# Optimization experiments

Measured on AMD Instinct MI355X. Metric: run time of the kernel, lower is better.

Reference implementation:

```python
import jax, jax.numpy as jnp
import numpy as np

B, N = 8192, 2048


def setup_inputs() -> dict:
    key = jax.random.key(0)
    k1, k2 = jax.random.split(key)
    predictions = jax.random.normal(k1, (B, N), dtype=jnp.float32)
    targets = jax.random.normal(k2, (B, N), dtype=jnp.float32)
    return {"predictions": predictions, "targets": targets}


def reference(predictions, targets):
    # Original: per-batch NxN squared-difference cost matrix + scipy Hungarian,
    # then MSE(pred, optimally-permuted targets), averaged over the batch.
    # For scalar entries with cost (p_i - t_j)^2 the optimal assignment is the
    # monotone matching (rearrangement inequality): sort both vectors and pair
    # in order. This computes the exact same loss, fully vectorized.
    p_sorted = jnp.sort(predictions, axis=-1)  # [B, N]
    t_sorted = jnp.sort(targets, axis=-1)      # [B, N]
    # mean over N per row, then mean over B == global mean
    return jnp.mean((p_sorted - t_sorted) ** 2)
```

## Files before the change

kernel.cpp:

```cpp
#include <hip/hip_runtime.h>
#include <math.h>

#define ROWS 8192
#define NCOL 2048
#define V 32
#define THREADS 256

__device__ __forceinline__ void ce(float& a, float& b) {
  const float lo = fminf(a, b);
  const float hi = fmaxf(a, b);
  a = lo; b = hi;
}

__device__ __forceinline__ float ce_dir(float a, float b, float cdir) {
  return __builtin_amdgcn_fmed3f(a, b, cdir);
}

template <int CTRL>
__device__ __forceinline__ float dpp_mov(float x) {
  return __builtin_bit_cast(
      float, __builtin_amdgcn_update_dpp(0, __builtin_bit_cast(int, x),
                                         CTRL, 0xF, 0xF, true));
}

template <int PAT>
__device__ __forceinline__ float swz(float x) {
  return __builtin_bit_cast(
      float, __builtin_amdgcn_ds_swizzle(__builtin_bit_cast(int, x), PAT));
}

template <int M>
__device__ __forceinline__ float lane_xor(float x, int a63) {
  if constexpr (M == 1)       return dpp_mov<0xB1>(x);
  else if constexpr (M == 2)  return dpp_mov<0x4E>(x);
  else if constexpr (M == 3)  return dpp_mov<0x1B>(x);
  else if constexpr (M == 7)  return dpp_mov<0x141>(x);
  else if constexpr (M == 8)  return dpp_mov<0x128>(x);
  else if constexpr (M == 15) return dpp_mov<0x140>(x);
  else if constexpr (M == 4)  return swz<0x101F>(x);
  else if constexpr (M == 16) return swz<0x401F>(x);
  else if constexpr (M == 31) return swz<0x7C1F>(x);
  else {
    return __builtin_bit_cast(
        float, __builtin_amdgcn_ds_bpermute(a63, __builtin_bit_cast(int, x)));
  }
}

template <int M>
__device__ __forceinline__ void xpass1(float (&x)[V], float cdir, int a63) {
#pragma unroll
  for (int c = 0; c < V; c += 8) {
    float o[8];
#pragma unroll
    for (int u = 0; u < 8; ++u) o[u] = lane_xor<M>(x[c + u], a63);
#pragma unroll
    for (int u = 0; u < 8; ++u) x[c + u] = ce_dir(x[c + u], o[u], cdir);
  }
}

template <int KB>
__device__ __forceinline__ void merge1(float (&x)[V], int lane, int a63) {
  {
    constexpr int LM = 2 * KB - 1;
    const float cdir = (lane & KB) ? INFINITY : -INFINITY;
#pragma unroll
    for (int q = 0; q < 4; ++q) {
      const int vA = 4 * q;
      float o[8];
#pragma unroll
      for (int u = 0; u < 4; ++u) {
        o[u]     = lane_xor<LM>(x[(vA + u) ^ 31], a63);
        o[u + 4] = lane_xor<LM>(x[vA + u], a63);
      }
#pragma unroll
      for (int u = 0; u < 4; ++u) {
        x[vA + u]        = ce_dir(x[vA + u],        o[u],     cdir);
        x[(vA + u) ^ 31] = ce_dir(x[(vA + u) ^ 31], o[u + 4], cdir);
      }
    }
  }
  if constexpr (KB >= 32) xpass1<16>(x, (lane & 16) ? INFINITY : -INFINITY, a63);
  if constexpr (KB >= 16) xpass1<8>(x, (lane & 8) ? INFINITY : -INFINITY, a63);
  if constexpr (KB >= 8)  xpass1<4>(x, (lane & 4) ? INFINITY : -INFINITY, a63);
  if constexpr (KB >= 4)  xpass1<2>(x, (lane & 2) ? INFINITY : -INFINITY, a63);
  if constexpr (KB >= 2)  xpass1<1>(x, (lane & 1) ? INFINITY : -INFINITY, a63);
#pragma unroll
  for (int j = 16; j >= 1; j >>= 1) {
#pragma unroll
    for (int v = 0; v < V; ++v) {
      if ((v & j) == 0) ce(x[v], x[v | j]);
    }
  }
}

__device__ __forceinline__ void sort_one(float (&x)[V], int lane, int a63) {
#pragma unroll
  for (int k = 2; k <= V; k <<= 1) {
#pragma unroll
    for (int v = 0; v < V; ++v) {
      if ((v & (k >> 1)) == 0) ce(x[v], x[v ^ (k - 1)]);
    }
#pragma unroll
    for (int j = k >> 2; j >= 1; j >>= 1) {
#pragma unroll
      for (int v = 0; v < V; ++v) {
        if ((v & j) == 0) ce(x[v], x[v | j]);
      }
    }
  }
  merge1<1>(x, lane, a63);
  merge1<2>(x, lane, a63);
  merge1<4>(x, lane, a63);
  merge1<8>(x, lane, a63);
  merge1<16>(x, lane, a63);
  merge1<32>(x, lane, a63);
}

__global__ __launch_bounds__(THREADS, 6) void sort_mse_kernel(
    const float* __restrict__ pred, const float* __restrict__ targ,
    float* __restrict__ out) {
  const int lane = threadIdx.x & 63;
  const int wave = threadIdx.x >> 6;
  const int pair = wave & 1;
  const int role = wave >> 1;
  const int row = blockIdx.x * 2 + pair;
  const size_t base = (size_t)row * NCOL + (size_t)lane * V;
  const int a63 = ((lane ^ 63) << 2);

  __shared__ float tbuf[2][NCOL];

  float x[V];
  const float4* s4 = (const float4*)((role ? targ : pred) + base);
#pragma unroll
  for (int q = 0; q < V / 4; ++q) {
    const float4 a = s4[q];
    x[4 * q + 0] = a.x; x[4 * q + 1] = a.y;
    x[4 * q + 2] = a.z; x[4 * q + 3] = a.w;
  }

  sort_one(x, lane, a63);

  if (role == 1) {
#pragma unroll
    for (int q = 0; q < V / 4; ++q) {
      const int w = lane * V + 4 * (q ^ (lane & 7));
      *(float4*)&tbuf[pair][w] =
          make_float4(x[4 * q + 0], x[4 * q + 1], x[4 * q + 2], x[4 * q + 3]);
    }
  }
  __syncthreads();
  if (role == 1) return;

  float acc = 0.f;
#pragma unroll
  for (int q = 0; q < V / 4; ++q) {
    const int w = lane * V + 4 * (q ^ (lane & 7));
    const float4 t4 = *(const float4*)&tbuf[pair][w];
    float d;
    d = x[4 * q + 0] - t4.x; acc = fmaf(d, d, acc);
    d = x[4 * q + 1] - t4.y; acc = fmaf(d, d, acc);
    d = x[4 * q + 2] - t4.z; acc = fmaf(d, d, acc);
    d = x[4 * q + 3] - t4.w; acc = fmaf(d, d, acc);
  }
#pragma unroll
  for (int off = 32; off > 0; off >>= 1) acc += __shfl_down(acc, off, 64);
  if (lane == 0) {
    unsafeAtomicAdd(out, acc * (1.0f / ((float)ROWS * (float)NCOL)));
  }
}

extern "C" void kernel_launch(void* const* d_in, const int* in_sizes, int n_in,
                              void* d_out, int out_size, void* d_ws, size_t ws_size,
                              hipStream_t stream) {
  const float* pred = (const float*)d_in[0];
  const float* targ = (const float*)d_in[1];
  float* out = (float*)d_out;

  hipMemsetAsync(out, 0, sizeof(float), stream);
  sort_mse_kernel<<<ROWS / 2, THREADS, 0, stream>>>(pred, targ, out);
}
```

Baseline: 233.4 us.

## Split each row sort across two waves with 16 values per lane

Each row is now sorted by two waves instead of one, so every lane holds 16 values rather than 32. The final cross-wave bitonic merge stage exchanges data through LDS, followed by lane-xor passes that include a new xor-32 bpermute. Grid size doubles to one row per block, and the launch bound rises to 8 to raise occupancy through lower register pressure. The cost is extra LDS traffic and an additional block barrier per row.

```diff
diff --git a/kernel.cpp b/kernel.cpp
--- a/kernel.cpp
+++ b/kernel.cpp
@@ -3,7 +3,7 @@
 
 #define ROWS 8192
 #define NCOL 2048
-#define V 32
+#define V 16
 #define THREADS 256
 
 __device__ __forceinline__ void ce(float& a, float& b) {
@@ -30,7 +30,7 @@
 }
 
 template <int M>
-__device__ __forceinline__ float lane_xor(float x, int a63) {
+__device__ __forceinline__ float lane_xor(float x, int a32, int a63) {
   if constexpr (M == 1)       return dpp_mov<0xB1>(x);
   else if constexpr (M == 2)  return dpp_mov<0x4E>(x);
   else if constexpr (M == 3)  return dpp_mov<0x1B>(x);
@@ -40,52 +40,57 @@
   else if constexpr (M == 4)  return swz<0x101F>(x);
   else if constexpr (M == 16) return swz<0x401F>(x);
   else if constexpr (M == 31) return swz<0x7C1F>(x);
-  else {
+  else if constexpr (M == 32) {
+    return __builtin_bit_cast(
+        float, __builtin_amdgcn_ds_bpermute(a32, __builtin_bit_cast(int, x)));
+  } else {
     return __builtin_bit_cast(
         float, __builtin_amdgcn_ds_bpermute(a63, __builtin_bit_cast(int, x)));
   }
 }
 
 template <int M>
-__device__ __forceinline__ void xpass1(float (&x)[V], float cdir, int a63) {
+__device__ __forceinline__ void xpass(float (&x)[V], float cdir,
+                                      int a32, int a63) {
 #pragma unroll
   for (int c = 0; c < V; c += 8) {
     float o[8];
 #pragma unroll
-    for (int u = 0; u < 8; ++u) o[u] = lane_xor<M>(x[c + u], a63);
+    for (int u = 0; u < 8; ++u) o[u] = lane_xor<M>(x[c + u], a32, a63);
 #pragma unroll
     for (int u = 0; u < 8; ++u) x[c + u] = ce_dir(x[c + u], o[u], cdir);
   }
 }
 
-template <int KB>
-__device__ __forceinline__ void merge1(float (&x)[V], int lane, int a63) {
+template <int S>
+__device__ __forceinline__ void mergeS(float (&x)[V], int lane,
+                                       int a32, int a63) {
   {
-    constexpr int LM = 2 * KB - 1;
-    const float cdir = (lane & KB) ? INFINITY : -INFINITY;
-#pragma unroll
-    for (int q = 0; q < 4; ++q) {
+    constexpr int LM = 2 * S - 1;
+    const float cdir = (lane & S) ? INFINITY : -INFINITY;
+#pragma unroll
+    for (int q = 0; q < 2; ++q) {
       const int vA = 4 * q;
       float o[8];
 #pragma unroll
       for (int u = 0; u < 4; ++u) {
-        o[u]     = lane_xor<LM>(x[(vA + u) ^ 31], a63);
-        o[u + 4] = lane_xor<LM>(x[vA + u], a63);
+        o[u]     = lane_xor<LM>(x[(vA + u) ^ 15], a32, a63);
+        o[u + 4] = lane_xor<LM>(x[vA + u], a32, a63);
       }
 #pragma unroll
       for (int u = 0; u < 4; ++u) {
         x[vA + u]        = ce_dir(x[vA + u],        o[u],     cdir);
-        x[(vA + u) ^ 31] = ce_dir(x[(vA + u) ^ 31], o[u + 4], cdir);
+        x[(vA + u) ^ 15] = ce_dir(x[(vA + u) ^ 15], o[u + 4], cdir);
       }
     }
   }
-  if constexpr (KB >= 32) xpass1<16>(x, (lane & 16) ? INFINITY : -INFINITY, a63);
-  if constexpr (KB >= 16) xpass1<8>(x, (lane & 8) ? INFINITY : -INFINITY, a63);
-  if constexpr (KB >= 8)  xpass1<4>(x, (lane & 4) ? INFINITY : -INFINITY, a63);
-  if constexpr (KB >= 4)  xpass1<2>(x, (lane & 2) ? INFINITY : -INFINITY, a63);
-  if constexpr (KB >= 2)  xpass1<1>(x, (lane & 1) ? INFINITY : -INFINITY, a63);
-#pragma unroll
-  for (int j = 16; j >= 1; j >>= 1) {
+  if constexpr (S >= 32) xpass<16>(x, (lane & 16) ? INFINITY : -INFINITY, a32, a63);
+  if constexpr (S >= 16) xpass<8>(x, (lane & 8) ? INFINITY : -INFINITY, a32, a63);
+  if constexpr (S >= 8)  xpass<4>(x, (lane & 4) ? INFINITY : -INFINITY, a32, a63);
+  if constexpr (S >= 4)  xpass<2>(x, (lane & 2) ? INFINITY : -INFINITY, a32, a63);
+  if constexpr (S >= 2)  xpass<1>(x, (lane & 1) ? INFINITY : -INFINITY, a32, a63);
+#pragma unroll
+  for (int j = 8; j >= 1; j >>= 1) {
 #pragma unroll
     for (int v = 0; v < V; ++v) {
       if ((v & j) == 0) ce(x[v], x[v | j]);
@@ -93,79 +98,114 @@
   }
 }
 
-__device__ __forceinline__ void sort_one(float (&x)[V], int lane, int a63) {
-#pragma unroll
-  for (int k = 2; k <= V; k <<= 1) {
-#pragma unroll
-    for (int v = 0; v < V; ++v) {
-      if ((v & (k >> 1)) == 0) ce(x[v], x[v ^ (k - 1)]);
-    }
-#pragma unroll
-    for (int j = k >> 2; j >= 1; j >>= 1) {
-#pragma unroll
-      for (int v = 0; v < V; ++v) {
-        if ((v & j) == 0) ce(x[v], x[v | j]);
-      }
-    }
-  }
-  merge1<1>(x, lane, a63);
-  merge1<2>(x, lane, a63);
-  merge1<4>(x, lane, a63);
-  merge1<8>(x, lane, a63);
-  merge1<16>(x, lane, a63);
-  merge1<32>(x, lane, a63);
-}
-
-__global__ __launch_bounds__(THREADS, 6) void sort_mse_kernel(
+__global__ __launch_bounds__(THREADS, 8) void sort_mse_kernel(
     const float* __restrict__ pred, const float* __restrict__ targ,
     float* __restrict__ out) {
   const int lane = threadIdx.x & 63;
   const int wave = threadIdx.x >> 6;
-  const int pair = wave & 1;
+  const int wp = wave & 1;
   const int role = wave >> 1;
-  const int row = blockIdx.x * 2 + pair;
-  const size_t base = (size_t)row * NCOL + (size_t)lane * V;
+  const int row = blockIdx.x;
+  const size_t base = (size_t)row * NCOL + (size_t)(wp * 64 + lane) * V;
+  const int a32 = ((lane ^ 32) << 2);
   const int a63 = ((lane ^ 63) << 2);
-
-  __shared__ float tbuf[2][NCOL];
+  const int swl = (lane ^ (lane >> 2)) & 3;
+
+  __shared__ float lds[4][64][V];
 
   float x[V];
   const float4* s4 = (const float4*)((role ? targ : pred) + base);
 #pragma unroll
-  for (int q = 0; q < V / 4; ++q) {
+  for (int q = 0; q < 4; ++q) {
     const float4 a = s4[q];
     x[4 * q + 0] = a.x; x[4 * q + 1] = a.y;
     x[4 * q + 2] = a.z; x[4 * q + 3] = a.w;
   }
 
-  sort_one(x, lane, a63);
-
+#pragma unroll
+  for (int k = 2; k <= V; k <<= 1) {
+#pragma unroll
+    for (int v = 0; v < V; ++v) {
+      if ((v & (k >> 1)) == 0) ce(x[v], x[v ^ (k - 1)]);
+    }
+#pragma unroll
+    for (int j = k >> 2; j >= 1; j >>= 1) {
+#pragma unroll
+      for (int v = 0; v < V; ++v) {
+        if ((v & j) == 0) ce(x[v], x[v | j]);
+      }
+    }
+  }
+
+  mergeS<1>(x, lane, a32, a63);
+  mergeS<2>(x, lane, a32, a63);
+  mergeS<4>(x, lane, a32, a63);
+  mergeS<8>(x, lane, a32, a63);
+  mergeS<16>(x, lane, a32, a63);
+  mergeS<32>(x, lane, a32, a63);
+
+#pragma unroll
+  for (int q = 0; q < 4; ++q) {
+    *(float4*)&lds[wave][lane][4 * (q ^ swl)] =
+        make_float4(x[4 * q + 0], x[4 * q + 1], x[4 * q + 2], x[4 * q + 3]);
+  }
+  __syncthreads();
+  {
+    const int ls = lane ^ 63;
+    const int swls = (ls ^ (ls >> 2)) & 3;
+    const float cdir64 = wp ? INFINITY : -INFINITY;
+    float4 t4[4];
+#pragma unroll
+    for (int q = 0; q < 4; ++q) {
+      t4[q] = *(const float4*)&lds[wave ^ 1][ls][4 * ((3 - q) ^ swls)];
+    }
+#pragma unroll
+    for (int q = 0; q < 4; ++q) {
+      x[4 * q + 0] = ce_dir(x[4 * q + 0], t4[q].w, cdir64);
+      x[4 * q + 1] = ce_dir(x[4 * q + 1], t4[q].z, cdir64);
+      x[4 * q + 2] = ce_dir(x[4 * q + 2], t4[q].y, cdir64);
+      x[4 * q + 3] = ce_dir(x[4 * q + 3], t4[q].x, cdir64);
+    }
+  }
+  xpass<32>(x, (lane & 32) ? INFINITY : -INFINITY, a32, a63);
+  xpass<16>(x, (lane & 16) ? INFINITY : -INFINITY, a32, a63);
+  xpass<8>(x, (lane & 8) ? INFINITY : -INFINITY, a32, a63);
+  xpass<4>(x, (lane & 4) ? INFINITY : -INFINITY, a32, a63);
+  xpass<2>(x, (lane & 2) ? INFINITY : -INFINITY, a32, a63);
+  xpass<1>(x, (lane & 1) ? INFINITY : -INFINITY, a32, a63);
+#pragma unroll
+  for (int j = 8; j >= 1; j >>= 1) {
+#pragma unroll
+    for (int v = 0; v < V; ++v) {
+      if ((v & j) == 0) ce(x[v], x[v | j]);
+    }
+  }
+
+  __syncthreads();
   if (role == 1) {
 #pragma unroll
-    for (int q = 0; q < V / 4; ++q) {
-      const int w = lane * V + 4 * (q ^ (lane & 7));
-      *(float4*)&tbuf[pair][w] =
+    for (int q = 0; q < 4; ++q) {
+      *(float4*)&lds[wave][lane][4 * (q ^ swl)] =
           make_float4(x[4 * q + 0], x[4 * q + 1], x[4 * q + 2], x[4 * q + 3]);
     }
   }
   __syncthreads();
-  if (role == 1) return;
-
-  float acc = 0.f;
-#pragma unroll
-  for (int q = 0; q < V / 4; ++q) {
-    const int w = lane * V + 4 * (q ^ (lane & 7));
-    const float4 t4 = *(const float4*)&tbuf[pair][w];
-    float d;
-    d = x[4 * q + 0] - t4.x; acc = fmaf(d, d, acc);
-    d = x[4 * q + 1] - t4.y; acc = fmaf(d, d, acc);
-    d = x[4 * q + 2] - t4.z; acc = fmaf(d, d, acc);
-    d = x[4 * q + 3] - t4.w; acc = fmaf(d, d, acc);
-  }
-#pragma unroll
-  for (int off = 32; off > 0; off >>= 1) acc += __shfl_down(acc, off, 64);
-  if (lane == 0) {
-    unsafeAtomicAdd(out, acc * (1.0f / ((float)ROWS * (float)NCOL)));
+  if (role == 0) {
+    float acc = 0.f;
+#pragma unroll
+    for (int q = 0; q < 4; ++q) {
+      const float4 t = *(const float4*)&lds[wave + 2][lane][4 * (q ^ swl)];
+      float d;
+      d = x[4 * q + 0] - t.x; acc = fmaf(d, d, acc);
+      d = x[4 * q + 1] - t.y; acc = fmaf(d, d, acc);
+      d = x[4 * q + 2] - t.z; acc = fmaf(d, d, acc);
+      d = x[4 * q + 3] - t.w; acc = fmaf(d, d, acc);
+    }
+#pragma unroll
+    for (int off = 32; off > 0; off >>= 1) acc += __shfl_down(acc, off, 64);
+    if (lane == 0) {
+      unsafeAtomicAdd(out, acc * (1.0f / ((float)ROWS * (float)NCOL)));
+    }
   }
 }
 
@@ -177,5 +217,5 @@
   float* out = (float*)d_out;
 
   hipMemsetAsync(out, 0, sizeof(float), stream);
-  sort_mse_kernel<<<ROWS / 2, THREADS, 0, stream>>>(pred, targ, out);
-}
+  sort_mse_kernel<<<ROWS, THREADS, 0, stream>>>(pred, targ, out);
+}
```

After: 327.9 us. +40.5%, slower.
